# Kernel optimization log

Hardware: AMD Instinct MI355X
Metric: run time of the kernel (lower is better)

The kernel has to match this reference:

```python
import jax, jax.numpy as jnp
import numpy as np

BATCH = 262144
NUM_LAYERS = 64


def setup_inputs() -> dict:
    key = jax.random.key(0)
    k1, k2, k3 = jax.random.split(key, 3)
    X = jax.random.normal(k1, (BATCH, 2), dtype=jnp.float32)
    weights = jax.random.normal(k2, (NUM_LAYERS, 3), dtype=jnp.float32)
    biases = jax.random.normal(k3, (NUM_LAYERS, 3), dtype=jnp.float32)
    return {"X": X, "weights": weights, "biases": biases}


def _unitaries(X, weights, biases):
    # Pad data with constant 1 -> [B, 3]
    Xp = jnp.concatenate([X, jnp.ones((X.shape[0], 1), X.dtype)], axis=1)
    # angles[b, k, l] = weights[l, k] * Xp[b, k] + biases[l, k]  -> [B, 3, L]
    angles = Xp[:, :, None] * weights.T[None, :, :] + biases.T[None, :, :]
    phi, theta, omega = angles[:, 0, :], angles[:, 1, :], angles[:, 2, :]  # [B, L]
    ct = jnp.cos(theta / 2)
    st = jnp.sin(theta / 2)
    ppo = (phi + omega) / 2
    pmo = (phi - omega) / 2
    m00 = jnp.exp(-1j * ppo) * ct
    m01 = -jnp.exp(1j * pmo) * st
    m10 = jnp.exp(-1j * pmo) * st
    m11 = jnp.exp(1j * ppo) * ct
    # [B, L, 2, 2] -> [L, B, 2, 2]
    M = jnp.stack([jnp.stack([m00, m01], axis=-1),
                   jnp.stack([m10, m11], axis=-1)], axis=-2)
    return jnp.transpose(M, (1, 0, 2, 3))


def reference(X, weights, biases):
    M = _unitaries(X, weights, biases)  # [L, B, 2, 2] complex64
    B = X.shape[0]
    s0 = jnp.tile(jnp.array([1.0 + 0.0j, 0.0 + 0.0j], dtype=M.dtype), (B, 1))  # |0>

    def step(s, u):  # s: [B, 2], u: [B, 2, 2]
        s = jnp.einsum('bij,bj->bi', u, s)
        return s, s

    _, states = jax.lax.scan(step, s0, M)  # [L, B, 2] complex64
    return states
```

## Files before the change

### kernel.cpp

```cpp
#include <hip/hip_runtime.h>

#define BATCH 262144
#define NUM_LAYERS 64

typedef float f32x2 __attribute__((ext_vector_type(2)));
typedef float f32x4 __attribute__((ext_vector_type(4)));

template <int MODE>
__global__ __launch_bounds__(256) void squbit_kernel(
    const float* __restrict__ X,
    const float* __restrict__ W,
    const float* __restrict__ Bi,
    float* __restrict__ out)
{
    __shared__ float4 cA[NUM_LAYERS];
    __shared__ float2 cOm[NUM_LAYERS];

    const int t = threadIdx.x;
    if (t < NUM_LAYERS) {
        const float w0 = W[t * 3 + 0], w1 = W[t * 3 + 1], w2 = W[t * 3 + 2];
        const float b0 = Bi[t * 3 + 0], b1 = Bi[t * 3 + 1], b2 = Bi[t * 3 + 2];
        float hom_prev = 0.0f;
        if (t > 0) hom_prev = 0.5f * (W[(t - 1) * 3 + 2] + Bi[(t - 1) * 3 + 2]);
        cA[t] = make_float4(0.5f * w0, fmaf(0.5f, b0, hom_prev), 0.5f * w1, 0.5f * b1);
        const float hom = 0.5f * (w2 + b2);
        float so, co;
        __sincosf(hom, &so, &co);
        cOm[t] = make_float2(co, so);
    }
    __syncthreads();

    const int b = blockIdx.x * 256 + t;
    const float2 x = reinterpret_cast<const float2*>(X)[b];

    f32x2 z = {1.0f, 0.0f};
    f32x2 w = {0.0f, 0.0f};

    f32x2* o2 = reinterpret_cast<f32x2*>(out);
    f32x4* o4 = reinterpret_cast<f32x4*>(out);

    #pragma unroll 4
    for (int l = 0; l < NUM_LAYERS; ++l) {
        const float4 c = cA[l];
        const float2 om = cOm[l];

        const float hpsi = fmaf(x.x, c.x, c.y);
        const float hth  = fmaf(x.y, c.z, c.w);

        float sps, cps, sth, cth;
        __sincosf(hpsi, &sps, &cps);
        __sincosf(hth,  &sth, &cth);

        const f32x2 nyw = {w.x, -w.y};
        const f32x2 nxz = {-z.x, z.y};
        const f32x2 az = z * cps + nyw * sps;
        const f32x2 aw = w * cps + nxz * sps;
        const f32x2 raz = {-az.y, az.x};
        const f32x2 raw = {-aw.y, aw.x};
        z = az * cth + raz * sth;
        w = aw * cth + raw * sth;

        const f32x2 nyw2 = {w.x, -w.y};
        const f32x2 zt = z * om.x + nyw2 * om.y;
        if (MODE == 0) {
            o2[l * BATCH + b] = zt;
        } else {
            const f32x2 nxz2 = {-z.x, z.y};
            const f32x2 wt = w * om.x + nxz2 * om.y;
            f32x4 v; v.x = zt.x; v.y = wt.x; v.z = zt.y; v.w = wt.y;
            o4[l * BATCH + b] = v;
        }
    }
}

extern "C" void kernel_launch(void* const* d_in, const int* in_sizes, int n_in,
                              void* d_out, int out_size, void* d_ws, size_t ws_size,
                              hipStream_t stream) {
    const float* X  = (const float*)d_in[0];
    const float* W  = (const float*)d_in[1];
    const float* Bi = (const float*)d_in[2];
    float* out = (float*)d_out;

    dim3 grid(BATCH / 256), block(256);

    const long long full_complex_floats = (long long)NUM_LAYERS * BATCH * 4;
    if ((long long)out_size >= full_complex_floats) {
        squbit_kernel<1><<<grid, block, 0, stream>>>(X, W, Bi, out);
    } else {
        squbit_kernel<0><<<grid, block, 0, stream>>>(X, W, Bi, out);
    }
}
```

Baseline: 28.82 us.

## Process four batch elements per thread with paired f32x2 state and wide stores

```diff
diff --git a/kernel.cpp b/kernel.cpp
--- a/kernel.cpp
+++ b/kernel.cpp
@@ -30,45 +30,94 @@
     }
     __syncthreads();
 
-    const int b = blockIdx.x * 256 + t;
-    const float2 x = reinterpret_cast<const float2*>(X)[b];
+    const int g  = blockIdx.x * 512 + t;
+    const int g2 = g + 256;
 
-    f32x2 z = {1.0f, 0.0f};
-    f32x2 w = {0.0f, 0.0f};
+    const float4 xxP = reinterpret_cast<const float4*>(X)[g];
+    const float4 xxQ = reinterpret_cast<const float4*>(X)[g2];
 
-    f32x2* o2 = reinterpret_cast<f32x2*>(out);
+    const f32x2 Px0 = {xxP.x, xxP.z}, Px1 = {xxP.y, xxP.w};
+    const f32x2 Qx0 = {xxQ.x, xxQ.z}, Qx1 = {xxQ.y, xxQ.w};
+
+    f32x2 Pur0 = {1.0f, 1.0f}, Pui0 = {0.0f, 0.0f};
+    f32x2 Pur1 = {0.0f, 0.0f}, Pui1 = {0.0f, 0.0f};
+    f32x2 Qur0 = {1.0f, 1.0f}, Qui0 = {0.0f, 0.0f};
+    f32x2 Qur1 = {0.0f, 0.0f}, Qui1 = {0.0f, 0.0f};
+
     f32x4* o4 = reinterpret_cast<f32x4*>(out);
 
-    #pragma unroll 4
+    #pragma unroll 2
     for (int l = 0; l < NUM_LAYERS; ++l) {
         const float4 c = cA[l];
         const float2 om = cOm[l];
 
-        const float hpsi = fmaf(x.x, c.x, c.y);
-        const float hth  = fmaf(x.y, c.z, c.w);
+        const f32x2 PhpsiV = Px0 * c.x + c.y;
+        const f32x2 PhthV  = Px1 * c.z + c.w;
+        const f32x2 QhpsiV = Qx0 * c.x + c.y;
+        const f32x2 QhthV  = Qx1 * c.z + c.w;
 
-        float sps, cps, sth, cth;
-        __sincosf(hpsi, &sps, &cps);
-        __sincosf(hth,  &sth, &cth);
+        float s0, c0, s1, c1, s2, c2, s3, c3;
+        float s4, c4, s5, c5, s6, c6, s7, c7;
+        __sincosf(PhpsiV.x, &s0, &c0);
+        __sincosf(PhpsiV.y, &s1, &c1);
+        __sincosf(PhthV.x,  &s2, &c2);
+        __sincosf(PhthV.y,  &s3, &c3);
+        __sincosf(QhpsiV.x, &s4, &c4);
+        __sincosf(QhpsiV.y, &s5, &c5);
+        __sincosf(QhthV.x,  &s6, &c6);
+        __sincosf(QhthV.y,  &s7, &c7);
+        const f32x2 Psps = {s0, s1}, Pcps = {c0, c1};
+        const f32x2 Psth = {s2, s3}, Pcth = {c2, c3};
+        const f32x2 Qsps = {s4, s5}, Qcps = {c4, c5};
+        const f32x2 Qsth = {s6, s7}, Qcth = {c6, c7};
 
-        const f32x2 nyw = {w.x, -w.y};
-        const f32x2 nxz = {-z.x, z.y};
-        const f32x2 az = z * cps + nyw * sps;
-        const f32x2 aw = w * cps + nxz * sps;
-        const f32x2 raz = {-az.y, az.x};
-        const f32x2 raw = {-aw.y, aw.x};
-        z = az * cth + raz * sth;
-        w = aw * cth + raw * sth;
+        {
+            const f32x2 a0r = Pui0 * Psps + Pur0 * Pcps;
+            const f32x2 a0i = Pui0 * Pcps - Pur0 * Psps;
+            const f32x2 a1r = Pur1 * Pcps - Pui1 * Psps;
+            const f32x2 a1i = Pui1 * Pcps + Pur1 * Psps;
+            Pur0 = Pcth * a0r - Psth * a1r;
+            Pui0 = Pcth * a0i - Psth * a1i;
+            Pur1 = Psth * a0r + Pcth * a1r;
+            Pui1 = Psth * a0i + Pcth * a1i;
+        }
+        {
+            const f32x2 a0r = Qui0 * Qsps + Qur0 * Qcps;
+            const f32x2 a0i = Qui0 * Qcps - Qur0 * Qsps;
+            const f32x2 a1r = Qur1 * Qcps - Qui1 * Qsps;
+            const f32x2 a1i = Qui1 * Qcps + Qur1 * Qsps;
+            Qur0 = Qcth * a0r - Qsth * a1r;
+            Qui0 = Qcth * a0i - Qsth * a1i;
+            Qur1 = Qsth * a0r + Qcth * a1r;
+            Qui1 = Qsth * a0i + Qcth * a1i;
+        }
 
-        const f32x2 nyw2 = {w.x, -w.y};
-        const f32x2 zt = z * om.x + nyw2 * om.y;
         if (MODE == 0) {
-            o2[l * BATCH + b] = zt;
+            const f32x2 Pt0r = Pui0 * om.y + Pur0 * om.x;
+            const f32x2 Pt1r = Pur1 * om.x - Pui1 * om.y;
+            const f32x2 Qt0r = Qui0 * om.y + Qur0 * om.x;
+            const f32x2 Qt1r = Qur1 * om.x - Qui1 * om.y;
+            f32x4 vp; vp.x = Pt0r.x; vp.y = Pt1r.x; vp.z = Pt0r.y; vp.w = Pt1r.y;
+            f32x4 vq; vq.x = Qt0r.x; vq.y = Qt1r.x; vq.z = Qt0r.y; vq.w = Qt1r.y;
+            o4[l * (BATCH / 2) + g]  = vp;
+            o4[l * (BATCH / 2) + g2] = vq;
         } else {
-            const f32x2 nxz2 = {-z.x, z.y};
-            const f32x2 wt = w * om.x + nxz2 * om.y;
-            f32x4 v; v.x = zt.x; v.y = wt.x; v.z = zt.y; v.w = wt.y;
-            o4[l * BATCH + b] = v;
+            const f32x2 Pt0r = Pui0 * om.y + Pur0 * om.x;
+            const f32x2 Pt0i = Pui0 * om.x - Pur0 * om.y;
+            const f32x2 Pt1r = Pur1 * om.x - Pui1 * om.y;
+            const f32x2 Pt1i = Pui1 * om.x + Pur1 * om.y;
+            const f32x2 Qt0r = Qui0 * om.y + Qur0 * om.x;
+            const f32x2 Qt0i = Qui0 * om.x - Qur0 * om.y;
+            const f32x2 Qt1r = Qur1 * om.x - Qui1 * om.y;
+            const f32x2 Qt1i = Qui1 * om.x + Qur1 * om.y;
+            f32x4 va; va.x = Pt0r.x; va.y = Pt0i.x; va.z = Pt1r.x; va.w = Pt1i.x;
+            f32x4 vb; vb.x = Pt0r.y; vb.y = Pt0i.y; vb.z = Pt1r.y; vb.w = Pt1i.y;
+            f32x4 vc; vc.x = Qt0r.x; vc.y = Qt0i.x; vc.z = Qt1r.x; vc.w = Qt1i.x;
+            f32x4 vd; vd.x = Qt0r.y; vd.y = Qt0i.y; vd.z = Qt1r.y; vd.w = Qt1i.y;
+            o4[(l * BATCH + 2 * g)  + 0] = va;
+            o4[(l * BATCH + 2 * g)  + 1] = vb;
+            o4[(l * BATCH + 2 * g2) + 0] = vc;
+            o4[(l * BATCH + 2 * g2) + 1] = vd;
         }
     }
 }
@@ -81,7 +130,7 @@
     const float* Bi = (const float*)d_in[2];
     float* out = (float*)d_out;
 
-    dim3 grid(BATCH / 256), block(256);
+    dim3 grid(BATCH / 1024), block(256);
 
     const long long full_complex_floats = (long long)NUM_LAYERS * BATCH * 4;
     if ((long long)out_size >= full_complex_floats) {
```

After: 27.12 us. 1.06x faster.
